# Performance work log

Measured on AMD Instinct MI355X. Metric: run time of the kernel, lower is better.

Reference implementation:

```python
import jax, jax.numpy as jnp
import numpy as np

N, D_IN, D, K = 8192, 1024, 256, 30
SCALE = D ** (-0.5)


def setup_inputs() -> dict:
    key = jax.random.key(0)
    ks = jax.random.split(key, 10)
    p = lambda k, sh: (jax.random.normal(k, sh, dtype=jnp.float32) * 0.02)
    return {
        'x_path': jax.random.normal(ks[0], (N, D_IN), dtype=jnp.float32),
        'W_fc1': p(ks[1], (D_IN, D)), 'b_fc1': jnp.zeros((D,), jnp.float32),
        'W_fc2': p(ks[2], (D, D)),   'b_fc2': jnp.zeros((D,), jnp.float32),
        'W_head': p(ks[3], (D, D)),  'b_head': jnp.zeros((D,), jnp.float32),
        'W_tail': p(ks[4], (D, D)),  'b_tail': jnp.zeros((D,), jnp.float32),
        'W_lin1': p(ks[5], (D, D)),  'b_lin1': jnp.zeros((D,), jnp.float32),
        'W_lin2': p(ks[6], (D, D)),  'b_lin2': jnp.zeros((D,), jnp.float32),
        'W_att1': p(ks[7], (D, D // 2)), 'b_att1': jnp.zeros((D // 2,), jnp.float32),
        'W_att2': p(ks[8], (D // 2, 1)), 'b_att2': jnp.zeros((1,), jnp.float32),
    }


def reference(x_path, W_fc1, b_fc1, W_fc2, b_fc2, W_head, b_head, W_tail, b_tail,
              W_lin1, b_lin1, W_lin2, b_lin2, W_att1, b_att1, W_att2, b_att2):
    # pathology_fc (eval mode, dropout = identity): 1024 -> 256 -> 256
    h = jax.nn.relu(x_path @ W_fc1 + b_fc1)
    h = jax.nn.relu(h @ W_fc2 + b_fc2)                      # [N, D]

    e_h = h @ W_head + b_head                               # [N, D]
    e_t = h @ W_tail + b_tail                               # [N, D]

    # pairwise scores + topk neighbor selection
    attn_logit = (e_h * SCALE) @ e_t.T                      # [N, N]
    topk_w, topk_i = jax.lax.top_k(attn_logit, K)           # [N, K]
    topk_prob = jax.nn.softmax(topk_w, axis=-1)             # [N, K]

    Nb_h = e_t[topk_i]                                      # gather neighbors [N, K, D]

    # gated message construction
    eh_r = topk_prob[..., None] * Nb_h + (1.0 - topk_prob)[..., None] * e_h[:, None, :]
    gate = jnp.tanh(e_h[:, None, :] + eh_r)                 # [N, K, D]

    # torch.einsum('ijkl,ijkm->ijk', Nb_h, gate): l and m summed independently
    ka_weight = Nb_h.sum(-1) * gate.sum(-1)                 # [N, K]
    ka_prob = jax.nn.softmax(ka_weight, axis=-1)            # [N, K]
    e_Nh = jnp.einsum('nk,nkd->nd', ka_prob, Nb_h)          # [N, D]

    sum_emb = jax.nn.relu((e_h + e_Nh) @ W_lin1 + b_lin1)
    bi_emb = jax.nn.relu((e_h * e_Nh) @ W_lin2 + b_lin2)
    e = sum_emb + bi_emb                                    # [N, D]

    # GlobalAttention readout
    att = jax.nn.leaky_relu(e @ W_att1 + b_att1, 0.01) @ W_att2 + b_att2   # [N, 1]
    a = jax.nn.softmax(att, axis=0)                         # softmax over nodes
    e_g = (a * e).sum(0)                                    # [D]
    return e, e_g
```

## Files before the change

kernel.cpp:

```cpp
#include <hip/hip_runtime.h>
#include <math.h>

#define NN   8192
#define DIN  1024
#define DD   256
#define TOPK 30
#define KP   40
#define CAP  88
#define NINF -3e38f

typedef short s8v  __attribute__((ext_vector_type(8)));
typedef float f16v __attribute__((ext_vector_type(16)));

__device__ __forceinline__ float wred_sum(float v) {
  v += __shfl_down(v, 32); v += __shfl_down(v, 16); v += __shfl_down(v, 8);
  v += __shfl_down(v, 4);  v += __shfl_down(v, 2);  v += __shfl_down(v, 1);
  return v;
}
__device__ __forceinline__ float wred_max(float v) {
  v = fmaxf(v, __shfl_down(v, 32)); v = fmaxf(v, __shfl_down(v, 16));
  v = fmaxf(v, __shfl_down(v, 8));  v = fmaxf(v, __shfl_down(v, 4));
  v = fmaxf(v, __shfl_down(v, 2));  v = fmaxf(v, __shfl_down(v, 1));
  return v;
}
__device__ __forceinline__ float tanh_fast(float x) {
  return 1.f - 2.f / (__expf(2.f * x) + 1.f);
}
__device__ __forceinline__ unsigned short f2bf(float x) {
  union { float f; unsigned int u; } v; v.f = x;
  unsigned int r = v.u + 0x7FFF + ((v.u >> 16) & 1);
  return (unsigned short)(r >> 16);
}
__device__ __forceinline__ bool pair_gt(float v, int i, float pv, int pi) {
  return (v > pv) || (v == pv && i < pi);
}
__device__ __forceinline__ unsigned key_pack(float f, int col) {
  unsigned b = __float_as_uint(f);
  unsigned u = ((int)b < 0) ? ~b : (b | 0x80000000u);
  return (u & 0xFFFFE000u) | (unsigned)col;
}

template<int ACT, int AOP, int ACCUM>
__global__ __launch_bounds__(128, 4)
void gemm_k(const float* __restrict__ A, const float* __restrict__ A2,
            const float* __restrict__ B, const float* __restrict__ bias,
            float* __restrict__ C, int K, int NB)
{
  __shared__ float sA[32 * 36];
  __shared__ float sB[32 * 68];
  const int t  = threadIdx.x;
  const int rb = blockIdx.x * 32;
  const int cb = blockIdx.y * 64;
  const int tr = t >> 4;
  const int tc = t & 15;

  float acc[4][4];
#pragma unroll
  for (int u = 0; u < 4; ++u)
#pragma unroll
    for (int j = 0; j < 4; ++j) acc[u][j] = 0.f;

  const int sr  = t >> 2;
  const int sk2 = (t & 3) * 4;

  for (int kt = 0; kt < K; kt += 32) {
    __syncthreads();
    {
      const float* Ap = A + (size_t)(rb + sr) * K + kt;
      float4 va = *(const float4*)(Ap + sk2);
      float4 vb = *(const float4*)(Ap + sk2 + 16);
      if (AOP) {
        const float* A2p = A2 + (size_t)(rb + sr) * K + kt;
        const float4 wa = *(const float4*)(A2p + sk2);
        const float4 wb = *(const float4*)(A2p + sk2 + 16);
        if (AOP == 1) {
          va.x += wa.x; va.y += wa.y; va.z += wa.z; va.w += wa.w;
          vb.x += wb.x; vb.y += wb.y; vb.z += wb.z; vb.w += wb.w;
        } else {
          va.x *= wa.x; va.y *= wa.y; va.z *= wa.z; va.w *= wa.w;
          vb.x *= wb.x; vb.y *= wb.y; vb.z *= wb.z; vb.w *= wb.w;
        }
      }
      sA[(sk2 + 0) * 36 + sr] = va.x; sA[(sk2 + 1) * 36 + sr] = va.y;
      sA[(sk2 + 2) * 36 + sr] = va.z; sA[(sk2 + 3) * 36 + sr] = va.w;
      sA[(sk2 + 16) * 36 + sr] = vb.x; sA[(sk2 + 17) * 36 + sr] = vb.y;
      sA[(sk2 + 18) * 36 + sr] = vb.z; sA[(sk2 + 19) * 36 + sr] = vb.w;
    }
    {
#pragma unroll
      for (int i = 0; i < 4; ++i) {
        const int f4 = t + 128 * i;
        const int k  = f4 >> 4;
        const int c4 = (f4 & 15) << 2;
        *(float4*)&sB[k * 68 + c4] = *(const float4*)&B[(size_t)(kt + k) * NB + cb + c4];
      }
    }
    __syncthreads();
#pragma unroll 8
    for (int k = 0; k < 32; ++k) {
      const float4 bv = *(const float4*)&sB[k * 68 + 4 * tc];
      const float4 av = *(const float4*)&sA[k * 36 + 4 * tr];
      const float a[4] = {av.x, av.y, av.z, av.w};
      const float b[4] = {bv.x, bv.y, bv.z, bv.w};
#pragma unroll
      for (int u = 0; u < 4; ++u)
#pragma unroll
        for (int j = 0; j < 4; ++j) acc[u][j] = fmaf(a[u], b[j], acc[u][j]);
    }
  }

  const float4 bz = *(const float4*)&bias[cb + 4 * tc];
  const float bb[4] = {bz.x, bz.y, bz.z, bz.w};
#pragma unroll
  for (int u = 0; u < 4; ++u) {
    const int row = rb + 4 * tr + u;
    float o[4];
#pragma unroll
    for (int j = 0; j < 4; ++j) {
      o[j] = acc[u][j] + bb[j];
      if (ACT) o[j] = fmaxf(o[j], 0.f);
    }
    float* Cp = &C[(size_t)row * NB + cb + 4 * tc];
    if (ACCUM) {
      const float4 old = *(const float4*)Cp;
      o[0] += old.x; o[1] += old.y; o[2] += old.z; o[3] += old.w;
    }
    float4 ov; ov.x = o[0]; ov.y = o[1]; ov.z = o[2]; ov.w = o[3];
    *(float4*)Cp = ov;
  }
}

__global__ __launch_bounds__(256)
void pack_frag_k(const float* __restrict__ src, unsigned short* __restrict__ dst)
{
  const int c = blockIdx.x * 256 + threadIdx.x;
  const int l = c & 63;
  const int W = (c >> 6) & 15;
  const int T = c >> 10;
  const int col = T * 32 + (l & 31);
  const int k0  = W * 16 + ((l >> 5) << 3);
  const float4 a = *(const float4*)&src[(size_t)col * DD + k0];
  const float4 b = *(const float4*)&src[(size_t)col * DD + k0 + 4];
  uint4 o;
  o.x = (unsigned)f2bf(a.x) | ((unsigned)f2bf(a.y) << 16);
  o.y = (unsigned)f2bf(a.z) | ((unsigned)f2bf(a.w) << 16);
  o.z = (unsigned)f2bf(b.x) | ((unsigned)f2bf(b.y) << 16);
  o.w = (unsigned)f2bf(b.z) | ((unsigned)f2bf(b.w) << 16);
  *(uint4*)&dst[(size_t)c * 8] = o;
}

__global__ __launch_bounds__(256)
void rowsum_k(const float* __restrict__ et, float* __restrict__ rs)
{
  const int t = threadIdx.x, lane = t & 63, w = t >> 6;
  const int n = blockIdx.x * 4 + w;
  const float4 v = *(const float4*)&et[(size_t)n * DD + lane * 4];
  float s = v.x + v.y + v.z + v.w;
  s = wred_sum(s);
  if (lane == 0) rs[n] = s;
}

__global__ __launch_bounds__(512, 4)
void score_cand_k(const unsigned short* __restrict__ ehF,
                  const unsigned short* __restrict__ etF,
                  unsigned* __restrict__ gCand)
{
  __shared__ unsigned sBuf[32 * CAP];
  __shared__ unsigned sK[32][KP];
  __shared__ unsigned sThrK[32];
  __shared__ int      sCnt[32];

  const int t = threadIdx.x, lane = t & 63, w = t >> 6;
  const int g  = blockIdx.x;
  const int sy = blockIdx.y;
  const int tile0 = sy * 128;
  const s8v* eh8 = (const s8v*)ehF;
  const s8v* et8 = (const s8v*)etF;

  s8v af[16];
#pragma unroll
  for (int W = 0; W < 16; ++W)
    af[W] = eh8[((size_t)g * 16 + W) * 64 + lane];

  for (int idx = t; idx < 32 * KP; idx += 512) ((unsigned*)sK)[idx] = 0u;
  if (t < 32) { sThrK[t] = 0u; sCnt[t] = 0; }
  __syncthreads();

  const int rq = 4 * (lane >> 5);
  const int colLane = lane & 31;
  const int leader = (lane >> 5) << 5;
  const unsigned lm = (1u << (lane & 31)) - 1;

  int tb = 0;
  for (int rnd = 0; rnd < 7; ++rnd) {
    const int ntile = (rnd == 0) ? 2 : (2 << (rnd - 1));
    unsigned thrv[16];
#pragma unroll
    for (int r = 0; r < 16; ++r) thrv[r] = sThrK[(r & 3) + 8 * (r >> 2) + rq];

    for (int p = w; p < ntile; p += 8) {
      const int T = tile0 + tb + p;
      const s8v* bp = et8 + (size_t)T * 1024 + lane;
      f16v c0, c1;
#pragma unroll
      for (int i = 0; i < 16; ++i) { c0[i] = 0.f; c1[i] = 0.f; }
      {
        s8v b[8];
#pragma unroll
        for (int q = 0; q < 8; ++q) b[q] = bp[q * 64];
#pragma unroll
        for (int q = 0; q < 8; ++q)
          c0 = __builtin_amdgcn_mfma_f32_32x32x16_bf16(af[q], b[q], c0, 0, 0, 0);
#pragma unroll
        for (int q = 0; q < 8; ++q) b[q] = bp[(8 + q) * 64];
#pragma unroll
        for (int q = 0; q < 8; ++q)
          c1 = __builtin_amdgcn_mfma_f32_32x32x16_bf16(af[8 + q], b[q], c1, 0, 0, 0);
      }
      const int col = T * 32 + colLane;
#pragma unroll
      for (int r = 0; r < 16; ++r) {
        const int row = (r & 3) + 8 * (r >> 2) + rq;
        const unsigned key = key_pack(c0[r] + c1[r], col);
        const bool pass = key > thrv[r];
        const unsigned long long mask = __ballot(pass);
        const unsigned hm = (unsigned)(mask >> leader);
        int base = 0;
        if ((lane & 31) == 0) base = atomicAdd(&sCnt[row], __popc(hm));
        base = __shfl(base, leader);
        if (pass) {
          const int ix = base + __popc(hm & lm);
          if (ix < CAP) sBuf[row * CAP + ix] = key;
        }
      }
    }
    __syncthreads();

#pragma unroll 1
    for (int rp = 0; rp < 2; ++rp) {
      const int ra = 4 * w + 2 * rp;
      const int rc = ra + 1;
      const int cA = min(sCnt[ra], CAP);
      const int cB = min(sCnt[rc], CAP);
      unsigned a0 = (lane < KP) ? sK[ra][lane]
                                : ((lane - KP) < cA ? sBuf[ra * CAP + (lane - KP)] : 0u);
      unsigned a1 = ((24 + lane) < cA) ? sBuf[ra * CAP + 24 + lane] : 0u;
      unsigned b0 = (lane < KP) ? sK[rc][lane]
                                : ((lane - KP) < cB ? sBuf[rc * CAP + (lane - KP)] : 0u);
      unsigned b1 = ((24 + lane) < cB) ? sBuf[rc * CAP + 24 + lane] : 0u;
#pragma unroll
      for (int k = 2; k <= 128; k <<= 1) {
#pragma unroll
        for (int j = k >> 1; j >= 1; j >>= 1) {
          if (j == 64) {
            unsigned mx = max(a0, a1), mn = min(a0, a1); a0 = mx; a1 = mn;
            mx = max(b0, b1); mn = min(b0, b1); b0 = mx; b1 = mn;
          } else {
            const unsigned pa0 = (unsigned)__shfl_xor((int)a0, j);
            const unsigned pa1 = (unsigned)__shfl_xor((int)a1, j);
            const unsigned pb0 = (unsigned)__shfl_xor((int)b0, j);
            const unsigned pb1 = (unsigned)__shfl_xor((int)b1, j);
            const bool km0 = (((lane & k) == 0)        == ((lane & j) == 0));
            const bool km1 = ((((64 + lane) & k) == 0) == ((lane & j) == 0));
            a0 = km0 ? max(a0, pa0) : min(a0, pa0);
            a1 = km1 ? max(a1, pa1) : min(a1, pa1);
            b0 = km0 ? max(b0, pb0) : min(b0, pb0);
            b1 = km1 ? max(b1, pb1) : min(b1, pb1);
          }
        }
      }
      if (rnd < 6) {
        if (lane < KP) { sK[ra][lane] = a0; sK[rc][lane] = b0; }
        if (lane == KP - 1) { sThrK[ra] = a0; sThrK[rc] = b0; }
        if (lane == 0) { sCnt[ra] = 0; sCnt[rc] = 0; }
      } else {
        if (lane < KP) {
          gCand[(((size_t)g * 2 + sy) * 32 + ra) * KP + lane] = a0;
          gCand[(((size_t)g * 2 + sy) * 32 + rc) * KP + lane] = b0;
        }
      }
    }
    __syncthreads();
    tb += ntile;
  }
}

__global__ __launch_bounds__(512, 2)
void cand_merge_k(const unsigned* __restrict__ gCand,
                  const float* __restrict__ e_h, const float* __restrict__ e_t,
                  float* __restrict__ topv_g, int* __restrict__ topi_g)
{
  __shared__ float    sEh[16 * 256];
  __shared__ unsigned sK40[16][KP];
  __shared__ float    sRes[16][KP];
  const int t = threadIdx.x, lane = t & 63, w = t >> 6;
  const int g = blockIdx.x, rb = g * 32;
  const int r0 = blockIdx.y * 16;

  for (int i = t; i < 1024; i += 512)
    ((float4*)sEh)[i] = ((const float4*)(e_h + (size_t)(rb + r0) * 256))[i];

#pragma unroll 1
  for (int rp = 0; rp < 2; ++rp) {
    const int lr = 2 * w + rp;
    const int r  = r0 + lr;
    unsigned v0, v1;
    {
      const int m = lane;
      const int s = m / 40, q = m - s * 40;
      v0 = gCand[(((size_t)g * 2 + s) * 32 + r) * KP + q];
    }
    {
      const int m = 64 + lane;
      if (m < 80) {
        const int q = m - 40;
        v1 = gCand[(((size_t)g * 2 + 1) * 32 + r) * KP + q];
      } else v1 = 0u;
    }
#pragma unroll
    for (int k = 2; k <= 128; k <<= 1) {
#pragma unroll
      for (int j = k >> 1; j >= 1; j >>= 1) {
        if (j == 64) {
          const unsigned mx = max(v0, v1), mn = min(v0, v1);
          v0 = mx; v1 = mn;
        } else {
          const unsigned p0 = (unsigned)__shfl_xor((int)v0, j);
          const unsigned p1 = (unsigned)__shfl_xor((int)v1, j);
          const bool km0 = (((lane & k) == 0)        == ((lane & j) == 0));
          const bool km1 = ((((64 + lane) & k) == 0) == ((lane & j) == 0));
          v0 = km0 ? max(v0, p0) : min(v0, p0);
          v1 = km1 ? max(v1, p1) : min(v1, p1);
        }
      }
    }
    if (lane < KP) sK40[lr][lane] = v0;
  }
  __syncthreads();

  for (int i = t; i < 16 * KP; i += 512) {
    const int lr = i / KP, q = i - lr * KP;
    const int c = (int)(sK40[lr][q] & 0x1FFFu);
    const float* et = &e_t[(size_t)c * 256];
    const float* eh = &sEh[lr * 256];
    float acc = 0.f;
#pragma unroll 8
    for (int d = 0; d < 64; ++d) {
      const float4 a = *(const float4*)&eh[d * 4];
      const float4 b = *(const float4*)&et[d * 4];
      acc = fmaf(a.x, b.x, acc); acc = fmaf(a.y, b.y, acc);
      acc = fmaf(a.z, b.z, acc); acc = fmaf(a.w, b.w, acc);
    }
    sRes[lr][q] = acc * 0.0625f;
  }
  __syncthreads();

#pragma unroll 1
  for (int rp = 0; rp < 2; ++rp) {
    const int lr = 2 * w + rp;
    float v; int c;
    if (lane < KP) { v = sRes[lr][lane]; c = (int)(sK40[lr][lane] & 0x1FFFu); }
    else           { v = NINF;           c = 0x40000000 + lane; }
#pragma unroll
    for (int k = 2; k <= 64; k <<= 1) {
#pragma unroll
      for (int j = k >> 1; j >= 1; j >>= 1) {
        const float pv = __shfl_xor(v, j);
        const int   pc = __shfl_xor(c, j);
        const bool km = (((lane & k) == 0) == ((lane & j) == 0));
        const bool gt = pair_gt(v, c, pv, pc);
        const bool keep = (km == gt);
        v = keep ? v : pv; c = keep ? c : pc;
      }
    }
    if (lane < TOPK) {
      topv_g[(size_t)(rb + r0 + lr) * TOPK + lane] = v;
      topi_g[(size_t)(rb + r0 + lr) * TOPK + lane] = c;
    }
  }
}

__global__ __launch_bounds__(256)
void message_k(const float* __restrict__ e_h, const float* __restrict__ e_t,
               const float* __restrict__ rs, const float* __restrict__ tv_g,
               const int* __restrict__ ti_g, float* __restrict__ e_Nh)
{
  __shared__ float sP[TOPK];
  __shared__ int   sI[TOPK];
  __shared__ float sW[TOPK];
  __shared__ float wpart[TOPK][4];
  const int n = blockIdx.x;
  const int t = threadIdx.x, lane = t & 63, w = t >> 6;

  if (w == 0) {
    const float v = (lane < TOPK) ? tv_g[(size_t)n * TOPK + lane] : NINF;
    float m = wred_max(v); m = __shfl(m, 0);
    const float p = (lane < TOPK) ? __expf(v - m) : 0.f;
    float s = wred_sum(p); s = __shfl(s, 0);
    if (lane < TOPK) { sP[lane] = p / s; sI[lane] = ti_g[(size_t)n * TOPK + lane]; }
  }
  __syncthreads();

  const float eh = e_h[(size_t)n * DD + t];
  float nbv[TOPK];
#pragma unroll
  for (int k = 0; k < TOPK; ++k) {
    const int   j = sI[k];
    const float p = sP[k];
    const float nb = e_t[(size_t)j * DD + t];
    nbv[k] = nb;
    float g = tanh_fast((2.f - p) * eh + p * nb);
    g = wred_sum(g);
    if (lane == 0) wpart[k][w] = g;
  }
  __syncthreads();

  if (w == 0) {
    float kw = NINF;
    if (lane < TOPK) {
      const float gs = wpart[lane][0] + wpart[lane][1] + wpart[lane][2] + wpart[lane][3];
      kw = rs[sI[lane]] * gs;
    }
    float m = wred_max(kw); m = __shfl(m, 0);
    const float p = (lane < TOPK) ? __expf(kw - m) : 0.f;
    float s = wred_sum(p); s = __shfl(s, 0);
    if (lane < TOPK) sW[lane] = p / s;
  }
  __syncthreads();

  float o = 0.f;
#pragma unroll
  for (int k = 0; k < TOPK; ++k) o = fmaf(sW[k], nbv[k], o);
  e_Nh[(size_t)n * DD + t] = o;
}

__global__ __launch_bounds__(256)
void att_k(const float* __restrict__ e, const float* __restrict__ W1,
           const float* __restrict__ b1, const float* __restrict__ W2,
           const float* __restrict__ b2, float* __restrict__ att)
{
  const int t = threadIdx.x;
  const int q = t >> 7;
  const int m = t & 127;
  const int lane = t & 63, w = t >> 6;
  const int n0 = blockIdx.x * 8 + q * 4;
  float acc[4] = {0.f, 0.f, 0.f, 0.f};
  for (int d = 0; d < DD; ++d) {
    const float wv = W1[d * 128 + m];
#pragma unroll
    for (int rr = 0; rr < 4; ++rr)
      acc[rr] = fmaf(e[(size_t)(n0 + rr) * DD + d], wv, acc[rr]);
  }
  const float b1m = b1[m], w2m = W2[m];
  __shared__ float part[4][4];
#pragma unroll
  for (int rr = 0; rr < 4; ++rr) {
    float v = acc[rr] + b1m;
    v = (v > 0.f) ? v : 0.01f * v;
    v *= w2m;
    v = wred_sum(v);
    if (lane == 0) part[w][rr] = v;
  }
  __syncthreads();
  if (t < 8) {
    const int qq = t >> 2, rr = t & 3;
    att[blockIdx.x * 8 + qq * 4 + rr] = part[qq * 2][rr] + part[qq * 2 + 1][rr] + b2[0];
  }
}

__global__ __launch_bounds__(1024)
void smax_prep_k(const float* __restrict__ att, float* __restrict__ stats,
                 float* __restrict__ eg)
{
  __shared__ float red[16];
  __shared__ float mg;
  const int t = threadIdx.x, lane = t & 63, w = t >> 6;
  float m = NINF;
#pragma unroll
  for (int i = 0; i < 8; ++i) m = fmaxf(m, att[t + 1024 * i]);
  m = wred_max(m);
  if (lane == 0) red[w] = m;
  __syncthreads();
  if (t == 0) {
    float mm = red[0];
    for (int i = 1; i < 16; ++i) mm = fmaxf(mm, red[i]);
    mg = mm;
  }
  __syncthreads();
  const float mm = mg;
  float s = 0.f;
#pragma unroll
  for (int i = 0; i < 8; ++i) s += __expf(att[t + 1024 * i] - mm);
  s = wred_sum(s);
  __syncthreads();
  if (lane == 0) red[w] = s;
  __syncthreads();
  if (t == 0) {
    float ss = 0.f;
    for (int i = 0; i < 16; ++i) ss += red[i];
    stats[0] = mm; stats[1] = ss;
  }
  if (t < DD) eg[t] = 0.f;
}

__global__ __launch_bounds__(256)
void eg_k(const float* __restrict__ att, const float* __restrict__ stats,
          const float* __restrict__ e, float* __restrict__ eg)
{
  const int t = threadIdx.x;
  const float m = stats[0], inv = 1.f / stats[1];
  float acc = 0.f;
  const int n0 = blockIdx.x * 128;
  for (int r = 0; r < 128; ++r) {
    const int n = n0 + r;
    acc = fmaf(__expf(att[n] - m), e[(size_t)n * DD + t], acc);
  }
  atomicAdd(&eg[t], acc * inv);
}

extern "C" void kernel_launch(void* const* d_in, const int* in_sizes, int n_in,
                              void* d_out, int out_size, void* d_ws, size_t ws_size,
                              hipStream_t stream)
{
  const float* x      = (const float*)d_in[0];
  const float* W_fc1  = (const float*)d_in[1];
  const float* b_fc1  = (const float*)d_in[2];
  const float* W_fc2  = (const float*)d_in[3];
  const float* b_fc2  = (const float*)d_in[4];
  const float* W_head = (const float*)d_in[5];
  const float* b_head = (const float*)d_in[6];
  const float* W_tail = (const float*)d_in[7];
  const float* b_tail = (const float*)d_in[8];
  const float* W_lin1 = (const float*)d_in[9];
  const float* b_lin1 = (const float*)d_in[10];
  const float* W_lin2 = (const float*)d_in[11];
  const float* b_lin2 = (const float*)d_in[12];
  const float* W_att1 = (const float*)d_in[13];
  const float* b_att1 = (const float*)d_in[14];
  const float* W_att2 = (const float*)d_in[15];
  const float* b_att2 = (const float*)d_in[16];

  float* out_e  = (float*)d_out;
  float* out_eg = out_e + (size_t)NN * DD;

  float* ws = (float*)d_ws;
  const size_t F = (size_t)NN * DD;
  float* e_h   = ws;
  float* e_t   = ws + F;
  float* e_Nh  = ws + 2 * F;
  float* bufA  = ws + 3 * F;
  float* bufB  = ws + 4 * F;
  float* rs    = ws + 5 * F;
  float* att   = rs + NN;
  float* stats = att + NN;
  float* topv  = stats + 16;
  int*   topi  = (int*)(topv + (size_t)NN * TOPK);

  unsigned short* ehF = (unsigned short*)bufA;
  unsigned short* etF = ehF + F;
  unsigned* gCand = (unsigned*)bufB;

  const dim3 blk(256);
  const dim3 gblk(128);
  const dim3 gemmGrid(NN / 32, DD / 64);

  gemm_k<1,0,0><<<gemmGrid, gblk, 0, stream>>>(x,    nullptr, W_fc1, b_fc1, bufA, DIN, DD);
  gemm_k<1,0,0><<<gemmGrid, gblk, 0, stream>>>(bufA, nullptr, W_fc2, b_fc2, bufB, DD,  DD);
  gemm_k<0,0,0><<<gemmGrid, gblk, 0, stream>>>(bufB, nullptr, W_head, b_head, e_h, DD, DD);
  gemm_k<0,0,0><<<gemmGrid, gblk, 0, stream>>>(bufB, nullptr, W_tail, b_tail, e_t, DD, DD);

  pack_frag_k<<<dim3(NN * DD / 8 / 256), blk, 0, stream>>>(e_h, ehF);
  pack_frag_k<<<dim3(NN * DD / 8 / 256), blk, 0, stream>>>(e_t, etF);
  rowsum_k<<<dim3(NN / 4), blk, 0, stream>>>(e_t, rs);

  score_cand_k<<<dim3(NN / 32, 2), dim3(512), 0, stream>>>(ehF, etF, gCand);
  cand_merge_k<<<dim3(NN / 32, 2), dim3(512), 0, stream>>>(gCand, e_h, e_t, topv, topi);

  message_k<<<dim3(NN), blk, 0, stream>>>(e_h, e_t, rs, topv, topi, e_Nh);

  gemm_k<1,1,0><<<gemmGrid, gblk, 0, stream>>>(e_h, e_Nh, W_lin1, b_lin1, out_e, DD, DD);
  gemm_k<1,2,1><<<gemmGrid, gblk, 0, stream>>>(e_h, e_Nh, W_lin2, b_lin2, out_e, DD, DD);

  att_k<<<dim3(NN / 8), blk, 0, stream>>>(out_e, W_att1, b_att1, W_att2, b_att2, att);
  smax_prep_k<<<dim3(1), dim3(1024), 0, stream>>>(att, stats, out_eg);
  eg_k<<<dim3(64), blk, 0, stream>>>(att, stats, out_e, out_eg);
}
```

Before: 727.4 us.

## Split candidate scoring into four column slices and widen merge bitonic sort

The score/candidate kernel now splits the key columns into four slices instead of two, running one fewer round per block and doubling the grid so more blocks run in parallel. The merge kernel now bitonic-sorts 160 candidates (four slices of 40) held as four registers per lane. The scoring loop also drops the dual accumulator and per-round cached thresholds, reading thresholds from shared memory on each check. The aim is better occupancy on the dominant top-k pass, at the cost of more candidate traffic and a larger merge sort.

Result: slower. 744.6 us (+2.4%).

```diff
diff --git a/kernel.cpp b/kernel.cpp
--- a/kernel.cpp
+++ b/kernel.cpp
@@ -7,6 +7,7 @@
 #define TOPK 30
 #define KP   40
 #define CAP  88
+#define NSL  4
 #define NINF -3e38f
 
 typedef short s8v  __attribute__((ext_vector_type(8)));
@@ -173,7 +174,7 @@
   const int t = threadIdx.x, lane = t & 63, w = t >> 6;
   const int g  = blockIdx.x;
   const int sy = blockIdx.y;
-  const int tile0 = sy * 128;
+  const int tile0 = sy * 64;
   const s8v* eh8 = (const s8v*)ehF;
   const s8v* et8 = (const s8v*)etF;
 
@@ -192,37 +193,33 @@
   const unsigned lm = (1u << (lane & 31)) - 1;
 
   int tb = 0;
-  for (int rnd = 0; rnd < 7; ++rnd) {
+  for (int rnd = 0; rnd < 6; ++rnd) {
     const int ntile = (rnd == 0) ? 2 : (2 << (rnd - 1));
-    unsigned thrv[16];
-#pragma unroll
-    for (int r = 0; r < 16; ++r) thrv[r] = sThrK[(r & 3) + 8 * (r >> 2) + rq];
-
     for (int p = w; p < ntile; p += 8) {
       const int T = tile0 + tb + p;
       const s8v* bp = et8 + (size_t)T * 1024 + lane;
-      f16v c0, c1;
-#pragma unroll
-      for (int i = 0; i < 16; ++i) { c0[i] = 0.f; c1[i] = 0.f; }
+      f16v c;
+#pragma unroll
+      for (int i = 0; i < 16; ++i) c[i] = 0.f;
       {
         s8v b[8];
 #pragma unroll
         for (int q = 0; q < 8; ++q) b[q] = bp[q * 64];
 #pragma unroll
         for (int q = 0; q < 8; ++q)
-          c0 = __builtin_amdgcn_mfma_f32_32x32x16_bf16(af[q], b[q], c0, 0, 0, 0);
+          c = __builtin_amdgcn_mfma_f32_32x32x16_bf16(af[q], b[q], c, 0, 0, 0);
 #pragma unroll
         for (int q = 0; q < 8; ++q) b[q] = bp[(8 + q) * 64];
 #pragma unroll
         for (int q = 0; q < 8; ++q)
-          c1 = __builtin_amdgcn_mfma_f32_32x32x16_bf16(af[8 + q], b[q], c1, 0, 0, 0);
+          c = __builtin_amdgcn_mfma_f32_32x32x16_bf16(af[8 + q], b[q], c, 0, 0, 0);
       }
       const int col = T * 32 + colLane;
 #pragma unroll
       for (int r = 0; r < 16; ++r) {
         const int row = (r & 3) + 8 * (r >> 2) + rq;
-        const unsigned key = key_pack(c0[r] + c1[r], col);
-        const bool pass = key > thrv[r];
+        const unsigned key = key_pack(c[r], col);
+        const bool pass = key > sThrK[row];
         const unsigned long long mask = __ballot(pass);
         const unsigned hm = (unsigned)(mask >> leader);
         int base = 0;
@@ -269,14 +266,14 @@
           }
         }
       }
-      if (rnd < 6) {
+      if (rnd < 5) {
         if (lane < KP) { sK[ra][lane] = a0; sK[rc][lane] = b0; }
         if (lane == KP - 1) { sThrK[ra] = a0; sThrK[rc] = b0; }
         if (lane == 0) { sCnt[ra] = 0; sCnt[rc] = 0; }
       } else {
         if (lane < KP) {
-          gCand[(((size_t)g * 2 + sy) * 32 + ra) * KP + lane] = a0;
-          gCand[(((size_t)g * 2 + sy) * 32 + rc) * KP + lane] = b0;
+          gCand[(((size_t)g * NSL + sy) * 32 + ra) * KP + lane] = a0;
+          gCand[(((size_t)g * NSL + sy) * 32 + rc) * KP + lane] = b0;
         }
       }
     }
@@ -304,37 +301,42 @@
   for (int rp = 0; rp < 2; ++rp) {
     const int lr = 2 * w + rp;
     const int r  = r0 + lr;
-    unsigned v0, v1;
-    {
-      const int m = lane;
-      const int s = m / 40, q = m - s * 40;
-      v0 = gCand[(((size_t)g * 2 + s) * 32 + r) * KP + q];
-    }
-    {
-      const int m = 64 + lane;
-      if (m < 80) {
-        const int q = m - 40;
-        v1 = gCand[(((size_t)g * 2 + 1) * 32 + r) * KP + q];
-      } else v1 = 0u;
-    }
-#pragma unroll
-    for (int k = 2; k <= 128; k <<= 1) {
+    unsigned v[4];
+#pragma unroll
+    for (int i = 0; i < 4; ++i) {
+      const int m = 64 * i + lane;
+      if (m < NSL * KP) {
+        const int s = m / KP, q = m - s * KP;
+        v[i] = gCand[(((size_t)g * NSL + s) * 32 + r) * KP + q];
+      } else v[i] = 0u;
+    }
+#pragma unroll
+    for (int k = 2; k <= 256; k <<= 1) {
 #pragma unroll
       for (int j = k >> 1; j >= 1; j >>= 1) {
-        if (j == 64) {
-          const unsigned mx = max(v0, v1), mn = min(v0, v1);
-          v0 = mx; v1 = mn;
+        if (j >= 64) {
+          const int di = j >> 6;
+#pragma unroll
+          for (int i = 0; i < 4; ++i) {
+            if (i & di) continue;
+            const int ii = i + di;
+            const bool descA = (((64 * i) & k) == 0);
+            const unsigned mx = max(v[i], v[ii]), mn = min(v[i], v[ii]);
+            v[i]  = descA ? mx : mn;
+            v[ii] = descA ? mn : mx;
+          }
         } else {
-          const unsigned p0 = (unsigned)__shfl_xor((int)v0, j);
-          const unsigned p1 = (unsigned)__shfl_xor((int)v1, j);
-          const bool km0 = (((lane & k) == 0)        == ((lane & j) == 0));
-          const bool km1 = ((((64 + lane) & k) == 0) == ((lane & j) == 0));
-          v0 = km0 ? max(v0, p0) : min(v0, p0);
-          v1 = km1 ? max(v1, p1) : min(v1, p1);
+#pragma unroll
+          for (int i = 0; i < 4; ++i) {
+            const unsigned p = (unsigned)__shfl_xor((int)v[i], j);
+            const bool desc = ((((64 * i) & k) | (lane & k)) == 0);
+            const bool km = (desc == ((lane & j) == 0));
+            v[i] = km ? max(v[i], p) : min(v[i], p);
+          }
         }
       }
     }
-    if (lane < KP) sK40[lr][lane] = v0;
+    if (lane < KP) sK40[lr][lane] = v[0];
   }
   __syncthreads();
 
@@ -573,7 +575,7 @@
   pack_frag_k<<<dim3(NN * DD / 8 / 256), blk, 0, stream>>>(e_t, etF);
   rowsum_k<<<dim3(NN / 4), blk, 0, stream>>>(e_t, rs);
 
-  score_cand_k<<<dim3(NN / 32, 2), dim3(512), 0, stream>>>(ehF, etF, gCand);
+  score_cand_k<<<dim3(NN / 32, NSL), dim3(512), 0, stream>>>(ehF, etF, gCand);
   cand_merge_k<<<dim3(NN / 32, 2), dim3(512), 0, stream>>>(gCand, e_h, e_t, topv, topi);
 
   message_k<<<dim3(NN), blk, 0, stream>>>(e_h, e_t, rs, topv, topi, e_Nh);
```
